# Kernel optimization log

Measured on AMD Instinct MI355X. Metric: run time of the kernel, lower is better.

The kernel has to match this reference:

```python
import jax, jax.numpy as jnp
import numpy as np

N, F_IN, H, HEADS = 50000, 128, 128, 4
C = H // HEADS
E = 800000


def layer_norm(x, w, b, eps=1e-5):
    mu = x.mean(-1, keepdims=True)
    var = ((x - mu) ** 2).mean(-1, keepdims=True)
    return (x - mu) * jax.lax.rsqrt(var + eps) * w + b


def gat_conv(x, src, dst, edge_attr, W, att_src, att_dst, W_edge, att_edge, bias):
    """PyG GATConv (concat=True, add_self_loops=True, fill_value='mean', edge_dim=H), eval mode."""
    n = x.shape[0]
    # self-loop edge_attr = mean of incoming edge attrs per node (PyG fill_value='mean')
    ones = jnp.ones((src.shape[0],), dtype=edge_attr.dtype)
    deg = jax.ops.segment_sum(ones, dst, n)
    loop_attr = jax.ops.segment_sum(edge_attr, dst, n) / jnp.maximum(deg, 1.0)[:, None]
    loop = jnp.arange(n, dtype=src.dtype)
    src = jnp.concatenate([src, loop])
    dst = jnp.concatenate([dst, loop])
    ea = jnp.concatenate([edge_attr, loop_attr], axis=0)  # [E+N, H]
    h = (x @ W).reshape(n, HEADS, C)                      # [N, heads, C]
    a_src = (h * att_src).sum(-1)                         # [N, heads]
    a_dst = (h * att_dst).sum(-1)
    e = (ea @ W_edge).reshape(-1, HEADS, C)
    a_edge = (e * att_edge).sum(-1)                       # [E+N, heads]
    alpha = jax.nn.leaky_relu(a_src[src] + a_dst[dst] + a_edge, 0.2)
    # segment softmax over destination neighborhoods
    m = jax.lax.stop_gradient(jax.ops.segment_max(alpha, dst, n))
    alpha = jnp.exp(alpha - m[dst])
    s = jax.ops.segment_sum(alpha, dst, n)
    alpha = alpha / (s[dst] + 1e-16)
    out = jax.ops.segment_sum(alpha[:, :, None] * h[src], dst, n)  # [N, heads, C]
    return out.reshape(n, H) + bias


def setup_inputs() -> dict:
    key = jax.random.key(0)
    ks = iter(jax.random.split(key, 40))
    def lin(k, i, o, s=0.05):
        return jax.random.normal(k, (i, o), jnp.float32) * s
    d = {}
    d["x"] = jax.random.normal(next(ks), (N, F_IN), jnp.float32)
    d["edge_time"] = jax.random.uniform(next(ks), (E,), jnp.float32)
    d["ip_w1"] = lin(next(ks), F_IN, 2 * H); d["ip_b1"] = jnp.zeros((2 * H,), jnp.float32)
    d["ip_ln_w"] = jnp.ones((2 * H,), jnp.float32); d["ip_ln_b"] = jnp.zeros((2 * H,), jnp.float32)
    d["ip_w2"] = lin(next(ks), 2 * H, H); d["ip_b2"] = jnp.zeros((H,), jnp.float32)
    d["pn_w"] = jnp.ones((H,), jnp.float32); d["pn_b"] = jnp.zeros((H,), jnp.float32)
    d["ta_w1"] = lin(next(ks), 1, H); d["ta_b1"] = jnp.zeros((H,), jnp.float32)
    d["ta_ln_w"] = jnp.ones((H,), jnp.float32); d["ta_ln_b"] = jnp.zeros((H,), jnp.float32)
    d["ta_w2"] = lin(next(ks), H, H); d["ta_b2"] = jnp.zeros((H,), jnp.float32)
    for p in ("g1", "g2"):
        d[p + "_w"] = lin(next(ks), H, H)
        d[p + "_att_src"] = jax.random.normal(next(ks), (HEADS, C), jnp.float32) * 0.05
        d[p + "_att_dst"] = jax.random.normal(next(ks), (HEADS, C), jnp.float32) * 0.05
        d[p + "_ew"] = lin(next(ks), H, H)
        d[p + "_att_edge"] = jax.random.normal(next(ks), (HEADS, C), jnp.float32) * 0.05
        d[p + "_b"] = jnp.zeros((H,), jnp.float32)
    d["n1_w"] = jnp.ones((H,), jnp.float32); d["n1_b"] = jnp.zeros((H,), jnp.float32)
    d["n2_w"] = jnp.ones((H,), jnp.float32); d["n2_b"] = jnp.zeros((H,), jnp.float32)
    d["edge_index"] = jax.random.randint(next(ks), (2, E), 0, N, jnp.int32)
    return d


def reference(x, edge_time, ip_w1, ip_b1, ip_ln_w, ip_ln_b, ip_w2, ip_b2, pn_w, pn_b,
              ta_w1, ta_b1, ta_ln_w, ta_ln_b, ta_w2, ta_b2,
              g1_w, g1_att_src, g1_att_dst, g1_ew, g1_att_edge, g1_b,
              g2_w, g2_att_src, g2_att_dst, g2_ew, g2_att_edge, g2_b,
              n1_w, n1_b, n2_w, n2_b, edge_index):
    src, dst = edge_index[0], edge_index[1]
    # input projection: Linear -> ReLU -> LayerNorm -> (Dropout eval) -> Linear
    h = jax.nn.relu(x @ ip_w1 + ip_b1)
    h = layer_norm(h, ip_ln_w, ip_ln_b)
    h = h @ ip_w2 + ip_b2
    h = jnp.clip(jax.nn.relu(layer_norm(h, pn_w, pn_b)), -10.0, 10.0)
    # temporal attention MLP on edge times -> per-edge edge_attr [E, H]
    tw = edge_time[:, None] @ ta_w1 + ta_b1
    tw = jax.nn.relu(layer_norm(tw, ta_ln_w, ta_ln_b))
    tw = jnp.clip(jnp.tanh(tw @ ta_w2 + ta_b2), -3.0, 3.0)
    # GAT layer 1 (single chunk => residual + clamp, mean over 1 chunk is identity)
    g = gat_conv(h, src, dst, tw, g1_w, g1_att_src, g1_att_dst, g1_ew, g1_att_edge, g1_b) + h
    g = jax.nn.elu(layer_norm(jnp.clip(g, -10.0, 10.0), n1_w, n1_b))
    # GAT layer 2
    g2 = gat_conv(g, src, dst, tw, g2_w, g2_att_src, g2_att_dst, g2_ew, g2_att_edge, g2_b) + g
    return jax.nn.elu(layer_norm(jnp.clip(g2, -10.0, 10.0), n2_w, n2_b))
```

## Files before the change

kernel.cpp:

```cpp
#include <hip/hip_runtime.h>

typedef unsigned short u16;
typedef __attribute__((ext_vector_type(8))) short bf8_t;
typedef __attribute__((ext_vector_type(4))) float f4_t;

constexpr int NN   = 50000;
constexpr int NE   = 800000;
constexpr int TBLN = 2048;
constexpr int MB64 = (NN + 63) / 64;
constexpr int FB   = NE / 256;

__device__ __forceinline__ u16 f2b(float f) {
  unsigned u = __float_as_uint(f);
  unsigned r = u + 0x7fffu + ((u >> 16) & 1u);
  return (u16)(r >> 16);
}
__device__ __forceinline__ u16 f2h(float f) {
  _Float16 h = (_Float16)f;
  return __builtin_bit_cast(unsigned short, h);
}
__device__ __forceinline__ float h2f(u16 v) {
  _Float16 h = __builtin_bit_cast(_Float16, v);
  return (float)h;
}
__device__ __forceinline__ unsigned packh(float a, float b) {
  return (unsigned)f2h(a) | ((unsigned)f2h(b) << 16);
}
__device__ __forceinline__ float blo(unsigned u) { return __uint_as_float(u << 16); }
__device__ __forceinline__ float bhi(unsigned u) { return __uint_as_float(u & 0xffff0000u); }
__device__ __forceinline__ float wred64(float v) {
#pragma unroll
  for (int o = 32; o; o >>= 1) v += __shfl_xor(v, o);
  return v;
}
__device__ __forceinline__ bf8_t ldv(const u16* p) { return *(const bf8_t*)p; }
__device__ __forceinline__ f4_t mfma16(bf8_t a, bf8_t b, f4_t c) {
  return __builtin_amdgcn_mfma_f32_16x16x32_bf16(a, b, c, 0, 0, 0);
}

__global__ __launch_bounds__(256) void prep_k(
    const float* __restrict__ ew1, const float* __restrict__ ate1,
    const float* __restrict__ ew2, const float* __restrict__ ate2,
    float* __restrict__ V,
    const float* __restrict__ w1, const float* __restrict__ w2,
    const float* __restrict__ gw1, const float* __restrict__ gw2,
    u16* __restrict__ w1t, u16* __restrict__ w2t,
    u16* __restrict__ g1wt, u16* __restrict__ g2wt,
    const int* __restrict__ dstv, int* __restrict__ deg,
    const float* __restrict__ x, u16* __restrict__ x16) {
  const int bid = blockIdx.x, t = threadIdx.x;
  if (bid == 0) {
#pragma unroll
    for (int rep = 0; rep < 2; ++rep) {
      int idx = t + rep * 256;
      int k = idx >> 2, hd = idx & 3;
      float s1 = 0.f, s2 = 0.f;
      for (int c = 0; c < 32; ++c) {
        s1 += ew1[k * 128 + hd * 32 + c] * ate1[hd * 32 + c];
        s2 += ew2[k * 128 + hd * 32 + c] * ate2[hd * 32 + c];
      }
      V[k * 8 + hd] = s1;
      V[k * 8 + 4 + hd] = s2;
    }
  } else if (bid <= 384) {
    int idx = (bid - 1) * 256 + t;
    if (idx < 32768) {
      int r = idx >> 8, c = idx & 255;
      w1t[c * 128 + r] = f2b(w1[idx]);
    } else if (idx < 65536) {
      int k = idx - 32768;
      int r = k >> 7, c = k & 127;
      w2t[c * 256 + r] = f2b(w2[k]);
    } else if (idx < 81920) {
      int k = idx - 65536;
      int r = k >> 7, c = k & 127;
      g1wt[c * 128 + r] = f2b(gw1[k]);
    } else {
      int k = idx - 81920;
      int r = k >> 7, c = k & 127;
      g2wt[c * 128 + r] = f2b(gw2[k]);
    }
  } else if (bid <= 384 + FB) {
    int e = (bid - 385) * 256 + t;
    if (e < NE) atomicAdd(&deg[dstv[e]], 1);
  } else {
    int idx = (bid - 385 - FB) * 256 + t;
    size_t e8 = (size_t)idx * 8;
    const float4 a = *(const float4*)(x + e8);
    const float4 b = *(const float4*)(x + e8 + 4);
    uint4 o;
    o.x = (unsigned)f2b(a.x) | ((unsigned)f2b(a.y) << 16);
    o.y = (unsigned)f2b(a.z) | ((unsigned)f2b(a.w) << 16);
    o.z = (unsigned)f2b(b.x) | ((unsigned)f2b(b.y) << 16);
    o.w = (unsigned)f2b(b.z) | ((unsigned)f2b(b.w) << 16);
    *(uint4*)(x16 + e8) = o;
  }
}

__global__ __launch_bounds__(128) void build_table(
    const float* __restrict__ taw1, const float* __restrict__ tab1,
    const float* __restrict__ talnw, const float* __restrict__ talnb,
    const float* __restrict__ taw2, const float* __restrict__ tab2,
    const float* __restrict__ V, float* __restrict__ tbl) {
  const int j = threadIdx.x;
  const int wv = j >> 6, ln = j & 63;
  const float t = (float)blockIdx.x / (float)(TBLN - 1);
  __shared__ float part[4];
  __shared__ float ush[128];
  __shared__ float pacc[16];
  float v = t * taw1[j] + tab1[j];
  float s = wred64(v), sq = wred64(v * v);
  if (ln == 0) { part[wv * 2] = s; part[wv * 2 + 1] = sq; }
  __syncthreads();
  float S = part[0] + part[2], SQ = part[1] + part[3];
  float mu = S * (1.f / 128.f);
  float var = SQ * (1.f / 128.f) - mu * mu;
  float rstd = rsqrtf(var + 1e-5f);
  float u = fmaxf((v - mu) * rstd * talnw[j] + talnb[j], 0.f);
  ush[j] = u;
  __syncthreads();
  float acc = 0.f;
  for (int k = 0; k < 128; ++k) acc += ush[k] * taw2[k * 128 + j];
  float w = tanhf(acc + tab2[j]);
  w = fminf(fmaxf(w, -3.f), 3.f);
#pragma unroll
  for (int p = 0; p < 8; ++p) {
    float z = wred64(w * V[j * 8 + p]);
    if (ln == 0) pacc[wv * 8 + p] = z;
  }
  __syncthreads();
  if (j < 8) tbl[blockIdx.x * 8 + j] = pacc[j] + pacc[8 + j];
}

__global__ __launch_bounds__(512) void scan1(const int* __restrict__ deg,
                                             int* __restrict__ indptr,
                                             int* __restrict__ blks) {
  const int t = threadIdx.x;
  const int i = blockIdx.x * 512 + t;
  int v = (i < NN) ? deg[i] : 0;
  const int lane = t & 63, wv = t >> 6;
  int x = v;
#pragma unroll
  for (int o = 1; o < 64; o <<= 1) {
    int y = __shfl_up(x, o);
    if (lane >= o) x += y;
  }
  __shared__ int ws[8];
  if (lane == 63) ws[wv] = x;
  __syncthreads();
  if (t < 8) {
    int y = ws[t];
#pragma unroll
    for (int o = 1; o < 8; o <<= 1) {
      int z = __shfl_up(y, o);
      if (t >= o) y += z;
    }
    ws[t] = y;
  }
  __syncthreads();
  int excl = wv ? ws[wv - 1] : 0;
  x += excl;
  if (i < NN) indptr[i + 1] = x;
  if (t == 511) blks[blockIdx.x] = x;
}
__global__ void scan2(int* __restrict__ blks, int nb) {
  const int t = threadIdx.x;
  int v = (t < nb) ? blks[t] : 0;
  const int lane = t & 63, wv = t >> 6;
  int x = v;
#pragma unroll
  for (int o = 1; o < 64; o <<= 1) {
    int y = __shfl_up(x, o);
    if (lane >= o) x += y;
  }
  __shared__ int ws[2];
  if (lane == 63) ws[wv] = x;
  __syncthreads();
  if (wv == 1) x += ws[0];
  if (t < nb) blks[t] = x - v;
}
__global__ __launch_bounds__(512) void scan3(int* __restrict__ indptr,
                                             const int* __restrict__ blks,
                                             const int* __restrict__ deg,
                                             int* __restrict__ cursor) {
  const int i = blockIdx.x * 512 + threadIdx.x;
  if (i < NN) {
    int v = indptr[i + 1] + blks[blockIdx.x];
    indptr[i + 1] = v;
    cursor[i] = v - deg[i];
  }
  if (i == 0) indptr[0] = 0;
}

__device__ void fill_body(int fb, const int* __restrict__ srcv,
                          const int* __restrict__ dstv,
                          const float* __restrict__ etime,
                          const float* __restrict__ tbl,
                          int* __restrict__ cursor,
                          u16* __restrict__ recs) {
  const int e = fb * 256 + threadIdx.x;
  if (e >= NE) return;
  int d = dstv[e];
  int pos = atomicAdd(&cursor[d], 1);
  float t = etime[e];
  t = fminf(fmaxf(t, 0.f), 1.f);
  float fpos = t * (float)(TBLN - 1);
  int i0 = (int)fpos;
  if (i0 > TBLN - 2) i0 = TBLN - 2;
  float fr = fpos - (float)i0;
  const float4* r = (const float4*)(tbl + i0 * 8);
  float4 a0 = r[0], a1 = r[1], b0 = r[2], b1 = r[3];
  float4 o1, o2;
  o1.x = a0.x + fr * (b0.x - a0.x); o1.y = a0.y + fr * (b0.y - a0.y);
  o1.z = a0.z + fr * (b0.z - a0.z); o1.w = a0.w + fr * (b0.w - a0.w);
  o2.x = a1.x + fr * (b1.x - a1.x); o2.y = a1.y + fr * (b1.y - a1.y);
  o2.z = a1.z + fr * (b1.z - a1.z); o2.w = a1.w + fr * (b1.w - a1.w);
  u16* rp = recs + (size_t)pos * 16;
  uint4 w;
  w.x = (unsigned)srcv[e];
  w.y = packh(o1.x, o1.y);
  w.z = packh(o1.z, o1.w);
  w.w = packh(o2.x, o2.y);
  *(uint4*)rp = w;
  *(unsigned*)(rp + 8) = packh(o2.z, o2.w);
}

__device__ void ip_body(int ipb, char* smem,
                        const u16* __restrict__ x16, const u16* __restrict__ w1t,
                        const float* __restrict__ b1, const float* __restrict__ ln1w,
                        const float* __restrict__ ln1b, const u16* __restrict__ w2t,
                        const float* __restrict__ b2, const float* __restrict__ pnw,
                        const float* __restrict__ pnb, u16* __restrict__ h16) {
  u16* h1n = (u16*)smem;
  u16* h2n = h1n;
  float* partS = (float*)(smem + 33792);
  float* partQ = (float*)(smem + 33792 + 1024);

  const int t = threadIdx.x;
  const int w = t >> 6, lane = t & 63, q = lane >> 4, l15 = lane & 15;
  const int rowbase = ipb * 64;

  f4_t acc[4][4];
#pragma unroll
  for (int mt = 0; mt < 4; ++mt)
#pragma unroll
    for (int nt = 0; nt < 4; ++nt) acc[mt][nt] = (f4_t){0.f, 0.f, 0.f, 0.f};
#pragma unroll
  for (int kst = 0; kst < 4; ++kst) {
    int k0 = kst * 32 + q * 8;
    bf8_t a[4];
#pragma unroll
    for (int mt = 0; mt < 4; ++mt) {
      int r = rowbase + mt * 16 + l15;
      if (r > NN - 1) r = NN - 1;
      a[mt] = ldv(x16 + (size_t)r * 128 + k0);
    }
#pragma unroll
    for (int nt = 0; nt < 4; ++nt) {
      int n = w * 64 + nt * 16 + l15;
      bf8_t b = ldv(w1t + n * 128 + k0);
#pragma unroll
      for (int mt = 0; mt < 4; ++mt)
        acc[mt][nt] = mfma16(a[mt], b, acc[mt][nt]);
    }
  }
#pragma unroll
  for (int nt = 0; nt < 4; ++nt) {
    float bb = b1[w * 64 + nt * 16 + l15];
#pragma unroll
    for (int mt = 0; mt < 4; ++mt)
#pragma unroll
      for (int r = 0; r < 4; ++r)
        acc[mt][nt][r] = fmaxf(acc[mt][nt][r] + bb, 0.f);
  }
  {
    float s[4][4], sq[4][4];
#pragma unroll
    for (int mt = 0; mt < 4; ++mt)
#pragma unroll
      for (int r = 0; r < 4; ++r) {
        float a0 = acc[mt][0][r], b0 = acc[mt][1][r], c0 = acc[mt][2][r], d0 = acc[mt][3][r];
        s[mt][r] = a0 + b0 + c0 + d0;
        sq[mt][r] = a0 * a0 + b0 * b0 + c0 * c0 + d0 * d0;
      }
#pragma unroll
    for (int o = 1; o < 16; o <<= 1)
#pragma unroll
      for (int mt = 0; mt < 4; ++mt)
#pragma unroll
        for (int r = 0; r < 4; ++r) {
          s[mt][r] += __shfl_xor(s[mt][r], o);
          sq[mt][r] += __shfl_xor(sq[mt][r], o);
        }
    if (l15 == 0) {
#pragma unroll
      for (int mt = 0; mt < 4; ++mt)
#pragma unroll
        for (int r = 0; r < 4; ++r) {
          int row = mt * 16 + q * 4 + r;
          partS[w * 64 + row] = s[mt][r];
          partQ[w * 64 + row] = sq[mt][r];
        }
    }
  }
  __syncthreads();
  {
    float lw[4], lb[4];
#pragma unroll
    for (int nt = 0; nt < 4; ++nt) {
      int col = w * 64 + nt * 16 + l15;
      lw[nt] = ln1w[col]; lb[nt] = ln1b[col];
    }
#pragma unroll
    for (int mt = 0; mt < 4; ++mt)
#pragma unroll
      for (int r = 0; r < 4; ++r) {
        int row = mt * 16 + q * 4 + r;
        float S = partS[row] + partS[64 + row] + partS[128 + row] + partS[192 + row];
        float Q = partQ[row] + partQ[64 + row] + partQ[128 + row] + partQ[192 + row];
        float mu = S * (1.f / 256.f);
        float var = Q * (1.f / 256.f) - mu * mu;
        float rstd = rsqrtf(var + 1e-5f);
#pragma unroll
        for (int nt = 0; nt < 4; ++nt) {
          int col = w * 64 + nt * 16 + l15;
          h1n[row * 264 + col] = f2b((acc[mt][nt][r] - mu) * rstd * lw[nt] + lb[nt]);
        }
      }
  }
  __syncthreads();
  f4_t acc2[4][2];
#pragma unroll
  for (int mt = 0; mt < 4; ++mt)
#pragma unroll
    for (int nt = 0; nt < 2; ++nt) acc2[mt][nt] = (f4_t){0.f, 0.f, 0.f, 0.f};
#pragma unroll
  for (int kst = 0; kst < 8; ++kst) {
    int k0 = kst * 32 + q * 8;
    bf8_t a[4];
#pragma unroll
    for (int mt = 0; mt < 4; ++mt)
      a[mt] = ldv(h1n + (mt * 16 + l15) * 264 + k0);
#pragma unroll
    for (int nt = 0; nt < 2; ++nt) {
      int n = w * 32 + nt * 16 + l15;
      bf8_t b = ldv(w2t + n * 256 + k0);
#pragma unroll
      for (int mt = 0; mt < 4; ++mt)
        acc2[mt][nt] = mfma16(a[mt], b, acc2[mt][nt]);
    }
  }
#pragma unroll
  for (int nt = 0; nt < 2; ++nt) {
    float bb = b2[w * 32 + nt * 16 + l15];
#pragma unroll
    for (int mt = 0; mt < 4; ++mt)
#pragma unroll
      for (int r = 0; r < 4; ++r)
        acc2[mt][nt][r] += bb;
  }
  {
    float s[4][4], sq[4][4];
#pragma unroll
    for (int mt = 0; mt < 4; ++mt)
#pragma unroll
      for (int r = 0; r < 4; ++r) {
        float a0 = acc2[mt][0][r], b0 = acc2[mt][1][r];
        s[mt][r] = a0 + b0;
        sq[mt][r] = a0 * a0 + b0 * b0;
      }
#pragma unroll
    for (int o = 1; o < 16; o <<= 1)
#pragma unroll
      for (int mt = 0; mt < 4; ++mt)
#pragma unroll
        for (int r = 0; r < 4; ++r) {
          s[mt][r] += __shfl_xor(s[mt][r], o);
          sq[mt][r] += __shfl_xor(sq[mt][r], o);
        }
    __syncthreads();
    if (l15 == 0) {
#pragma unroll
      for (int mt = 0; mt < 4; ++mt)
#pragma unroll
        for (int r = 0; r < 4; ++r) {
          int row = mt * 16 + q * 4 + r;
          partS[w * 64 + row] = s[mt][r];
          partQ[w * 64 + row] = sq[mt][r];
        }
    }
  }
  __syncthreads();
  {
    float lw[2], lb[2];
#pragma unroll
    for (int nt = 0; nt < 2; ++nt) {
      int col = w * 32 + nt * 16 + l15;
      lw[nt] = pnw[col]; lb[nt] = pnb[col];
    }
#pragma unroll
    for (int mt = 0; mt < 4; ++mt)
#pragma unroll
      for (int r = 0; r < 4; ++r) {
        int row = mt * 16 + q * 4 + r;
        float S = partS[row] + partS[64 + row] + partS[128 + row] + partS[192 + row];
        float Q = partQ[row] + partQ[64 + row] + partQ[128 + row] + partQ[192 + row];
        float mu = S * (1.f / 128.f);
        float var = Q * (1.f / 128.f) - mu * mu;
        float rstd = rsqrtf(var + 1e-5f);
#pragma unroll
        for (int nt = 0; nt < 2; ++nt) {
          int col = w * 32 + nt * 16 + l15;
          float v = (acc2[mt][nt][r] - mu) * rstd * lw[nt] + lb[nt];
          v = fminf(fmaxf(v, 0.f), 10.f);
          h2n[row * 128 + col] = f2b(v);
        }
      }
  }
  __syncthreads();
  {
    const int row = t >> 2, cb = (t & 3) * 32;
    int rg = rowbase + row;
    if (rg < NN) {
#pragma unroll
      for (int c = 0; c < 4; ++c) {
        uint4 v0 = *(const uint4*)(h2n + row * 128 + cb + c * 8);
        *(uint4*)(h16 + (size_t)rg * 128 + cb + c * 8) = v0;
      }
    }
  }
}

__global__ __launch_bounds__(256) void fillip_k(
    const int* srcv, const int* dstv, const float* etime, const float* tbl,
    int* cursor, u16* recs,
    const u16* x16, const u16* w1t, const float* b1, const float* ln1w,
    const float* ln1b, const u16* w2t, const float* b2, const float* pnw,
    const float* pnb, u16* h16) {
  __shared__ char smem[35840];
  const int bid = blockIdx.x;
  if (bid % 5 == 0) {
    ip_body(bid / 5, smem, x16, w1t, b1, ln1w, ln1b, w2t, b2, pnw, pnb, h16);
  } else {
    fill_body(bid - bid / 5 - 1, srcv, dstv, etime, tbl, cursor, recs);
  }
}

__global__ __launch_bounds__(256) void hp_mfma(
    const u16* __restrict__ feat16, const u16* __restrict__ wt,
    const float* __restrict__ attsrc, const float* __restrict__ attdst,
    u16* __restrict__ hp16, float* __restrict__ asrc, float* __restrict__ adst) {
  const int t = threadIdx.x;
  const int w = t >> 6, lane = t & 63, q = lane >> 4, l15 = lane & 15;
  const int rowbase = blockIdx.x * 64;
  f4_t acc[4][2];
#pragma unroll
  for (int mt = 0; mt < 4; ++mt)
#pragma unroll
    for (int nt = 0; nt < 2; ++nt) acc[mt][nt] = (f4_t){0.f, 0.f, 0.f, 0.f};
#pragma unroll
  for (int kst = 0; kst < 4; ++kst) {
    int k0 = kst * 32 + q * 8;
    bf8_t a[4];
#pragma unroll
    for (int mt = 0; mt < 4; ++mt) {
      int r = rowbase + mt * 16 + l15;
      if (r > NN - 1) r = NN - 1;
      a[mt] = ldv(feat16 + (size_t)r * 128 + k0);
    }
#pragma unroll
    for (int nt = 0; nt < 2; ++nt) {
      int n = w * 32 + nt * 16 + l15;
      bf8_t b = ldv(wt + n * 128 + k0);
#pragma unroll
      for (int mt = 0; mt < 4; ++mt)
        acc[mt][nt] = mfma16(a[mt], b, acc[mt][nt]);
    }
  }
  float ps[4][4], pd[4][4];
#pragma unroll
  for (int mt = 0; mt < 4; ++mt)
#pragma unroll
    for (int r = 0; r < 4; ++r) { ps[mt][r] = 0.f; pd[mt][r] = 0.f; }
#pragma unroll
  for (int mt = 0; mt < 4; ++mt)
#pragma unroll
    for (int nt = 0; nt < 2; ++nt) {
      int col = w * 32 + nt * 16 + l15;
      float as = attsrc[col], ad = attdst[col];
#pragma unroll
      for (int r = 0; r < 4; ++r) {
        int row = mt * 16 + q * 4 + r;
        int rg = rowbase + row;
        float v = acc[mt][nt][r];
        if (rg < NN) hp16[(size_t)rg * 128 + col] = f2b(v);
        ps[mt][r] += v * as;
        pd[mt][r] += v * ad;
      }
    }
#pragma unroll
  for (int o = 1; o < 16; o <<= 1)
#pragma unroll
    for (int mt = 0; mt < 4; ++mt)
#pragma unroll
      for (int r = 0; r < 4; ++r) {
        ps[mt][r] += __shfl_xor(ps[mt][r], o);
        pd[mt][r] += __shfl_xor(pd[mt][r], o);
      }
  if (l15 == 0) {
#pragma unroll
    for (int mt = 0; mt < 4; ++mt)
#pragma unroll
      for (int r = 0; r < 4; ++r) {
        int rg = rowbase + mt * 16 + q * 4 + r;
        if (rg < NN) {
          asrc[rg * 4 + w] = ps[mt][r];
          adst[rg * 4 + w] = pd[mt][r];
        }
      }
  }
}

template <int L, int FINAL>
__global__ __launch_bounds__(256) void agg_k(
    const int* __restrict__ indptr, const u16* __restrict__ recs,
    const float* __restrict__ asrc, const float* __restrict__ adst,
    const u16* __restrict__ hp16, const u16* __restrict__ feat16,
    const float* __restrict__ gbias, const float* __restrict__ lnw,
    const float* __restrict__ lnb, u16* __restrict__ gout16,
    float* __restrict__ out32) {
  const int wv = threadIdx.x >> 6, lane = threadIdx.x & 63;
  const int n = blockIdx.x * 4 + wv;
  if (n >= NN) return;
  const int s0 = indptr[n], s1 = indptr[n + 1];
  const int dg = s1 - s0;
  const int g = lane >> 4, sl = lane & 15, cb = sl * 8, hdB = sl >> 2;
  const float advB = adst[n * 4 + hdB];
  float ssp = 0.f, sap = 0.f;
  float acc[8];
#pragma unroll
  for (int i = 0; i < 8; ++i) acc[i] = 0.f;
  for (int base = s0; base < s1; base += 8) {
    int i0 = base + g, i1 = base + 4 + g;
    int j0 = i0 < s1 ? i0 : s1 - 1;
    int j1 = i1 < s1 ? i1 : s1 - 1;
    const u16* r0 = recs + (size_t)j0 * 16;
    const u16* r1 = recs + (size_t)j1 * 16;
    int sc0 = *(const int*)r0, sc1 = *(const int*)r1;
    float ae0 = h2f(r0[2 + 4 * L + hdB]);
    float ae1v = h2f(r1[2 + 4 * L + hdB]);
    float as0 = asrc[sc0 * 4 + hdB], as1 = asrc[sc1 * 4 + hdB];
    const uint4 row0 = *(const uint4*)(hp16 + (size_t)sc0 * 128 + cb);
    const uint4 row1 = *(const uint4*)(hp16 + (size_t)sc1 * 128 + cb);
    float l0 = as0 + advB + ae0; l0 = fmaxf(l0, 0.2f * l0);
    float l1 = as1 + advB + ae1v; l1 = fmaxf(l1, 0.2f * l1);
    float w0 = (i0 < s1) ? __expf(l0) : 0.f;
    float w1 = (i1 < s1) ? __expf(l1) : 0.f;
    ssp += w0 + w1;
    sap += ((i0 < s1) ? ae0 : 0.f) + ((i1 < s1) ? ae1v : 0.f);
    acc[0] += w0 * blo(row0.x) + w1 * blo(row1.x);
    acc[1] += w0 * bhi(row0.x) + w1 * bhi(row1.x);
    acc[2] += w0 * blo(row0.y) + w1 * blo(row1.y);
    acc[3] += w0 * bhi(row0.y) + w1 * bhi(row1.y);
    acc[4] += w0 * blo(row0.z) + w1 * blo(row1.z);
    acc[5] += w0 * bhi(row0.z) + w1 * bhi(row1.z);
    acc[6] += w0 * blo(row0.w) + w1 * blo(row1.w);
    acc[7] += w0 * bhi(row0.w) + w1 * bhi(row1.w);
  }
#pragma unroll
  for (int i = 0; i < 8; ++i) {
    acc[i] += __shfl_xor(acc[i], 16);
    acc[i] += __shfl_xor(acc[i], 32);
  }
  ssp += __shfl_xor(ssp, 16); ssp += __shfl_xor(ssp, 32);
  sap += __shfl_xor(sap, 16); sap += __shfl_xor(sap, 32);
  const float degf = (float)(dg > 0 ? dg : 1);
  float asnB = asrc[n * 4 + hdB];
  float la = asnB + advB + sap / degf;
  la = fmaxf(la, 0.2f * la);
  float wsf = __expf(la);
  float inv = 1.f / (ssp + wsf + 1e-16f);
  const uint4 rs4 = *(const uint4*)(hp16 + (size_t)n * 128 + cb);
  const uint4 rr4 = *(const uint4*)(feat16 + (size_t)n * 128 + cb);
  const float4 gb0 = *(const float4*)(gbias + cb);
  const float4 gb1 = *(const float4*)(gbias + cb + 4);
  float v[8];
  v[0] = (acc[0] + wsf * blo(rs4.x)) * inv + gb0.x + blo(rr4.x);
  v[1] = (acc[1] + wsf * bhi(rs4.x)) * inv + gb0.y + bhi(rr4.x);
  v[2] = (acc[2] + wsf * blo(rs4.y)) * inv + gb0.z + blo(rr4.y);
  v[3] = (acc[3] + wsf * bhi(rs4.y)) * inv + gb0.w + bhi(rr4.y);
  v[4] = (acc[4] + wsf * blo(rs4.z)) * inv + gb1.x + blo(rr4.z);
  v[5] = (acc[5] + wsf * bhi(rs4.z)) * inv + gb1.y + bhi(rr4.z);
  v[6] = (acc[6] + wsf * blo(rs4.w)) * inv + gb1.z + blo(rr4.w);
  v[7] = (acc[7] + wsf * bhi(rs4.w)) * inv + gb1.w + bhi(rr4.w);
  float sum = 0.f, sq = 0.f;
#pragma unroll
  for (int i = 0; i < 8; ++i) {
    v[i] = fminf(fmaxf(v[i], -10.f), 10.f);
    sum += v[i]; sq += v[i] * v[i];
  }
#pragma unroll
  for (int o = 1; o < 16; o <<= 1) {
    sum += __shfl_xor(sum, o);
    sq += __shfl_xor(sq, o);
  }
  float mu = sum * (1.f / 128.f);
  float var = sq * (1.f / 128.f) - mu * mu;
  float rstd = rsqrtf(var + 1e-5f);
  const float4 lw0 = *(const float4*)(lnw + cb);
  const float4 lw1 = *(const float4*)(lnw + cb + 4);
  const float4 lb0 = *(const float4*)(lnb + cb);
  const float4 lb1 = *(const float4*)(lnb + cb + 4);
  float y[8];
  y[0] = (v[0] - mu) * rstd * lw0.x + lb0.x;
  y[1] = (v[1] - mu) * rstd * lw0.y + lb0.y;
  y[2] = (v[2] - mu) * rstd * lw0.z + lb0.z;
  y[3] = (v[3] - mu) * rstd * lw0.w + lb0.w;
  y[4] = (v[4] - mu) * rstd * lw1.x + lb1.x;
  y[5] = (v[5] - mu) * rstd * lw1.y + lb1.y;
  y[6] = (v[6] - mu) * rstd * lw1.z + lb1.z;
  y[7] = (v[7] - mu) * rstd * lw1.w + lb1.w;
#pragma unroll
  for (int i = 0; i < 8; ++i) y[i] = y[i] > 0.f ? y[i] : expm1f(y[i]);
  if (g == 0) {
    if (FINAL) {
      float4 o0 = {y[0], y[1], y[2], y[3]};
      float4 o1 = {y[4], y[5], y[6], y[7]};
      *(float4*)(out32 + (size_t)n * 128 + cb) = o0;
      *(float4*)(out32 + (size_t)n * 128 + cb + 4) = o1;
    } else {
      uint4 o;
      o.x = (unsigned)f2b(y[0]) | ((unsigned)f2b(y[1]) << 16);
      o.y = (unsigned)f2b(y[2]) | ((unsigned)f2b(y[3]) << 16);
      o.z = (unsigned)f2b(y[4]) | ((unsigned)f2b(y[5]) << 16);
      o.w = (unsigned)f2b(y[6]) | ((unsigned)f2b(y[7]) << 16);
      *(uint4*)(gout16 + (size_t)n * 128 + cb) = o;
    }
  }
}

extern "C" void kernel_launch(void* const* d_in, const int* in_sizes, int n_in,
                              void* d_out, int out_size, void* d_ws, size_t ws_size,
                              hipStream_t stream) {
  const float* x      = (const float*)d_in[0];
  const float* etime  = (const float*)d_in[1];
  const float* ip_w1  = (const float*)d_in[2];
  const float* ip_b1  = (const float*)d_in[3];
  const float* ip_lnw = (const float*)d_in[4];
  const float* ip_lnb = (const float*)d_in[5];
  const float* ip_w2  = (const float*)d_in[6];
  const float* ip_b2  = (const float*)d_in[7];
  const float* pn_w   = (const float*)d_in[8];
  const float* pn_b   = (const float*)d_in[9];
  const float* ta_w1  = (const float*)d_in[10];
  const float* ta_b1  = (const float*)d_in[11];
  const float* ta_lnw = (const float*)d_in[12];
  const float* ta_lnb = (const float*)d_in[13];
  const float* ta_w2  = (const float*)d_in[14];
  const float* ta_b2  = (const float*)d_in[15];
  const float* g1_w   = (const float*)d_in[16];
  const float* g1_as  = (const float*)d_in[17];
  const float* g1_ad  = (const float*)d_in[18];
  const float* g1_ew  = (const float*)d_in[19];
  const float* g1_ae  = (const float*)d_in[20];
  const float* g1_b   = (const float*)d_in[21];
  const float* g2_w   = (const float*)d_in[22];
  const float* g2_as  = (const float*)d_in[23];
  const float* g2_ad  = (const float*)d_in[24];
  const float* g2_ew  = (const float*)d_in[25];
  const float* g2_ae  = (const float*)d_in[26];
  const float* g2_b   = (const float*)d_in[27];
  const float* n1_w   = (const float*)d_in[28];
  const float* n1_b   = (const float*)d_in[29];
  const float* n2_w   = (const float*)d_in[30];
  const float* n2_b   = (const float*)d_in[31];
  const int* eidx     = (const int*)d_in[32];
  const int* srcv = eidx;
  const int* dstv = eidx + NE;

  char* p = (char*)d_ws;
  auto carve = [&](size_t bytes) -> char* {
    char* r = p;
    p += (bytes + 255) & ~(size_t)255;
    return r;
  };
  u16*   h16    = (u16*)carve((size_t)NN * 128 * 2);
  u16*   g16    = (u16*)carve((size_t)NN * 128 * 2);
  u16*   hp16   = (u16*)carve((size_t)NN * 128 * 2);
  float* asrc   = (float*)carve((size_t)NN * 4 * 4);
  float* adst   = (float*)carve((size_t)NN * 4 * 4);
  u16*   recs   = (u16*)carve((size_t)NE * 32);
  int*   deg    = (int*)carve((size_t)NN * 4);
  int*   indptr = (int*)carve((size_t)(NN + 1) * 4);
  int*   cursor = (int*)carve((size_t)NN * 4);
  int*   blks   = (int*)carve(512 * 4);
  float* V      = (float*)carve(128 * 8 * 4);
  float* tbl    = (float*)carve((size_t)TBLN * 8 * 4);
  u16*   w1t    = (u16*)carve(128 * 256 * 2);
  u16*   w2t    = (u16*)carve(256 * 128 * 2);
  u16*   g1wt   = (u16*)carve(128 * 128 * 2);
  u16*   g2wt   = (u16*)carve(128 * 128 * 2);
  u16*   x16    = (u16*)g16;

  hipMemsetAsync(deg, 0, (size_t)NN * 4, stream);

  const int SCB = (NN + 511) / 512;

  prep_k<<<1 + 384 + FB + FB, 256, 0, stream>>>(g1_ew, g1_ae, g2_ew, g2_ae, V,
                                                ip_w1, ip_w2, g1_w, g2_w,
                                                w1t, w2t, g1wt, g2wt, dstv, deg,
                                                x, x16);
  build_table<<<TBLN, 128, 0, stream>>>(ta_w1, ta_b1, ta_lnw, ta_lnb, ta_w2, ta_b2, V, tbl);
  scan1<<<SCB, 512, 0, stream>>>(deg, indptr, blks);
  scan2<<<1, 128, 0, stream>>>(blks, SCB);
  scan3<<<SCB, 512, 0, stream>>>(indptr, blks, deg, cursor);
  fillip_k<<<MB64 + FB, 256, 0, stream>>>(srcv, dstv, etime, tbl, cursor, recs,
                                          x16, w1t, ip_b1, ip_lnw, ip_lnb, w2t, ip_b2,
                                          pn_w, pn_b, h16);
  hp_mfma<<<MB64, 256, 0, stream>>>(h16, g1wt, g1_as, g1_ad, hp16, asrc, adst);
  agg_k<0, 0><<<NN / 4, 256, 0, stream>>>(indptr, recs, asrc, adst, hp16, h16,
                                          g1_b, n1_w, n1_b, g16, nullptr);
  hp_mfma<<<MB64, 256, 0, stream>>>(g16, g2wt, g2_as, g2_ad, hp16, asrc, adst);
  agg_k<1, 1><<<NN / 4, 256, 0, stream>>>(indptr, recs, asrc, adst, hp16, g16,
                                          g2_b, n2_w, n2_b, nullptr, (float*)d_out);
}
```

Before: 389.7 us.

## Fuse GAT linear projections into input-projection and layer-1 aggregation kernels

Removes both standalone hp_mfma launches. The layer-1 projection (h·W1 plus the attention logits) now runs as MFMA inside the input-projection blocks, reading h from shared memory whose row stride is padded to 136 elements. The layer-2 projection is computed per node inside the layer-1 aggregation kernel with scalar FMAs and a butterfly shuffle reduction, writing to separate hp16b/asrc2/adst2 buffers. This saves two launches and the re-read of h and g from global memory, but adds heavy scalar ALU and weight-load work per node (each wave loads a 128x128 weight tile) inside the latency-bound aggregation kernel.

Result: slower. 406.9 us (+4.4%).

```diff
diff --git a/kernel.cpp b/kernel.cpp
--- a/kernel.cpp
+++ b/kernel.cpp
@@ -230,7 +230,10 @@
                         const float* __restrict__ b1, const float* __restrict__ ln1w,
                         const float* __restrict__ ln1b, const u16* __restrict__ w2t,
                         const float* __restrict__ b2, const float* __restrict__ pnw,
-                        const float* __restrict__ pnb, u16* __restrict__ h16) {
+                        const float* __restrict__ pnb, u16* __restrict__ h16,
+                        const u16* __restrict__ g1wt, const float* __restrict__ attsrc,
+                        const float* __restrict__ attdst, u16* __restrict__ hp16,
+                        float* __restrict__ asrc, float* __restrict__ adst) {
   u16* h1n = (u16*)smem;
   u16* h2n = h1n;
   float* partS = (float*)(smem + 33792);
@@ -413,7 +416,7 @@
           int col = w * 32 + nt * 16 + l15;
           float v = (acc2[mt][nt][r] - mu) * rstd * lw[nt] + lb[nt];
           v = fminf(fmaxf(v, 0.f), 10.f);
-          h2n[row * 128 + col] = f2b(v);
+          h2n[row * 136 + col] = f2b(v);
         }
       }
   }
@@ -424,9 +427,74 @@
     if (rg < NN) {
 #pragma unroll
       for (int c = 0; c < 4; ++c) {
-        uint4 v0 = *(const uint4*)(h2n + row * 128 + cb + c * 8);
+        uint4 v0 = *(const uint4*)(h2n + row * 136 + cb + c * 8);
         *(uint4*)(h16 + (size_t)rg * 128 + cb + c * 8) = v0;
       }
+    }
+  }
+  f4_t acc3[4][2];
+#pragma unroll
+  for (int mt = 0; mt < 4; ++mt)
+#pragma unroll
+    for (int nt = 0; nt < 2; ++nt) acc3[mt][nt] = (f4_t){0.f, 0.f, 0.f, 0.f};
+#pragma unroll
+  for (int kst = 0; kst < 4; ++kst) {
+    int k0 = kst * 32 + q * 8;
+    bf8_t a[4];
+#pragma unroll
+    for (int mt = 0; mt < 4; ++mt)
+      a[mt] = ldv(h2n + (mt * 16 + l15) * 136 + k0);
+#pragma unroll
+    for (int nt = 0; nt < 2; ++nt) {
+      int n = w * 32 + nt * 16 + l15;
+      bf8_t b = ldv(g1wt + n * 128 + k0);
+#pragma unroll
+      for (int mt = 0; mt < 4; ++mt)
+        acc3[mt][nt] = mfma16(a[mt], b, acc3[mt][nt]);
+    }
+  }
+  {
+    float ps[4][4], pd[4][4];
+#pragma unroll
+    for (int mt = 0; mt < 4; ++mt)
+#pragma unroll
+      for (int r = 0; r < 4; ++r) { ps[mt][r] = 0.f; pd[mt][r] = 0.f; }
+#pragma unroll
+    for (int mt = 0; mt < 4; ++mt)
+#pragma unroll
+      for (int nt = 0; nt < 2; ++nt) {
+        int col = w * 32 + nt * 16 + l15;
+        float as = attsrc[col], ad = attdst[col];
+#pragma unroll
+        for (int r = 0; r < 4; ++r) {
+          int row = mt * 16 + q * 4 + r;
+          int rg = rowbase + row;
+          float v = acc3[mt][nt][r];
+          if (rg < NN) hp16[(size_t)rg * 128 + col] = f2b(v);
+          ps[mt][r] += v * as;
+          pd[mt][r] += v * ad;
+        }
+      }
+#pragma unroll
+    for (int o = 1; o < 16; o <<= 1)
+#pragma unroll
+      for (int mt = 0; mt < 4; ++mt)
+#pragma unroll
+        for (int r = 0; r < 4; ++r) {
+          ps[mt][r] += __shfl_xor(ps[mt][r], o);
+          pd[mt][r] += __shfl_xor(pd[mt][r], o);
+        }
+    if (l15 == 0) {
+#pragma unroll
+      for (int mt = 0; mt < 4; ++mt)
+#pragma unroll
+        for (int r = 0; r < 4; ++r) {
+          int rg = rowbase + mt * 16 + q * 4 + r;
+          if (rg < NN) {
+            asrc[rg * 4 + w] = ps[mt][r];
+            adst[rg * 4 + w] = pd[mt][r];
+          }
+        }
     }
   }
 }
@@ -436,88 +504,16 @@
     int* cursor, u16* recs,
     const u16* x16, const u16* w1t, const float* b1, const float* ln1w,
     const float* ln1b, const u16* w2t, const float* b2, const float* pnw,
-    const float* pnb, u16* h16) {
+    const float* pnb, u16* h16,
+    const u16* g1wt, const float* g1as, const float* g1ad,
+    u16* hp16, float* asrc, float* adst) {
   __shared__ char smem[35840];
   const int bid = blockIdx.x;
   if (bid % 5 == 0) {
-    ip_body(bid / 5, smem, x16, w1t, b1, ln1w, ln1b, w2t, b2, pnw, pnb, h16);
+    ip_body(bid / 5, smem, x16, w1t, b1, ln1w, ln1b, w2t, b2, pnw, pnb, h16,
+            g1wt, g1as, g1ad, hp16, asrc, adst);
   } else {
     fill_body(bid - bid / 5 - 1, srcv, dstv, etime, tbl, cursor, recs);
-  }
-}
-
-__global__ __launch_bounds__(256) void hp_mfma(
-    const u16* __restrict__ feat16, const u16* __restrict__ wt,
-    const float* __restrict__ attsrc, const float* __restrict__ attdst,
-    u16* __restrict__ hp16, float* __restrict__ asrc, float* __restrict__ adst) {
-  const int t = threadIdx.x;
-  const int w = t >> 6, lane = t & 63, q = lane >> 4, l15 = lane & 15;
-  const int rowbase = blockIdx.x * 64;
-  f4_t acc[4][2];
-#pragma unroll
-  for (int mt = 0; mt < 4; ++mt)
-#pragma unroll
-    for (int nt = 0; nt < 2; ++nt) acc[mt][nt] = (f4_t){0.f, 0.f, 0.f, 0.f};
-#pragma unroll
-  for (int kst = 0; kst < 4; ++kst) {
-    int k0 = kst * 32 + q * 8;
-    bf8_t a[4];
-#pragma unroll
-    for (int mt = 0; mt < 4; ++mt) {
-      int r = rowbase + mt * 16 + l15;
-      if (r > NN - 1) r = NN - 1;
-      a[mt] = ldv(feat16 + (size_t)r * 128 + k0);
-    }
-#pragma unroll
-    for (int nt = 0; nt < 2; ++nt) {
-      int n = w * 32 + nt * 16 + l15;
-      bf8_t b = ldv(wt + n * 128 + k0);
-#pragma unroll
-      for (int mt = 0; mt < 4; ++mt)
-        acc[mt][nt] = mfma16(a[mt], b, acc[mt][nt]);
-    }
-  }
-  float ps[4][4], pd[4][4];
-#pragma unroll
-  for (int mt = 0; mt < 4; ++mt)
-#pragma unroll
-    for (int r = 0; r < 4; ++r) { ps[mt][r] = 0.f; pd[mt][r] = 0.f; }
-#pragma unroll
-  for (int mt = 0; mt < 4; ++mt)
-#pragma unroll
-    for (int nt = 0; nt < 2; ++nt) {
-      int col = w * 32 + nt * 16 + l15;
-      float as = attsrc[col], ad = attdst[col];
-#pragma unroll
-      for (int r = 0; r < 4; ++r) {
-        int row = mt * 16 + q * 4 + r;
-        int rg = rowbase + row;
-        float v = acc[mt][nt][r];
-        if (rg < NN) hp16[(size_t)rg * 128 + col] = f2b(v);
-        ps[mt][r] += v * as;
-        pd[mt][r] += v * ad;
-      }
-    }
-#pragma unroll
-  for (int o = 1; o < 16; o <<= 1)
-#pragma unroll
-    for (int mt = 0; mt < 4; ++mt)
-#pragma unroll
-      for (int r = 0; r < 4; ++r) {
-        ps[mt][r] += __shfl_xor(ps[mt][r], o);
-        pd[mt][r] += __shfl_xor(pd[mt][r], o);
-      }
-  if (l15 == 0) {
-#pragma unroll
-    for (int mt = 0; mt < 4; ++mt)
-#pragma unroll
-      for (int r = 0; r < 4; ++r) {
-        int rg = rowbase + mt * 16 + q * 4 + r;
-        if (rg < NN) {
-          asrc[rg * 4 + w] = ps[mt][r];
-          adst[rg * 4 + w] = pd[mt][r];
-        }
-      }
   }
 }
 
@@ -528,7 +524,10 @@
     const u16* __restrict__ hp16, const u16* __restrict__ feat16,
     const float* __restrict__ gbias, const float* __restrict__ lnw,
     const float* __restrict__ lnb, u16* __restrict__ gout16,
-    float* __restrict__ out32) {
+    float* __restrict__ out32,
+    const u16* __restrict__ g2wt, const float* __restrict__ as2,
+    const float* __restrict__ ad2, u16* __restrict__ hp16b,
+    float* __restrict__ asrc2, float* __restrict__ adst2) {
   const int wv = threadIdx.x >> 6, lane = threadIdx.x & 63;
   const int n = blockIdx.x * 4 + wv;
   if (n >= NN) return;
@@ -622,19 +621,81 @@
   y[7] = (v[7] - mu) * rstd * lw1.w + lb1.w;
 #pragma unroll
   for (int i = 0; i < 8; ++i) y[i] = y[i] > 0.f ? y[i] : expm1f(y[i]);
-  if (g == 0) {
-    if (FINAL) {
+  if (FINAL) {
+    if (g == 0) {
       float4 o0 = {y[0], y[1], y[2], y[3]};
       float4 o1 = {y[4], y[5], y[6], y[7]};
       *(float4*)(out32 + (size_t)n * 128 + cb) = o0;
       *(float4*)(out32 + (size_t)n * 128 + cb + 4) = o1;
-    } else {
+    }
+  } else {
+    if (g == 0) {
       uint4 o;
       o.x = (unsigned)f2b(y[0]) | ((unsigned)f2b(y[1]) << 16);
       o.y = (unsigned)f2b(y[2]) | ((unsigned)f2b(y[3]) << 16);
       o.z = (unsigned)f2b(y[4]) | ((unsigned)f2b(y[5]) << 16);
       o.w = (unsigned)f2b(y[6]) | ((unsigned)f2b(y[7]) << 16);
       *(uint4*)(gout16 + (size_t)n * 128 + cb) = o;
+    }
+    float t0[16], t1[16];
+#pragma unroll
+    for (int c = 0; c < 16; ++c) {
+      const uint4 a4 = *(const uint4*)(g2wt + (g * 32 + c) * 128 + cb);
+      const uint4 b4 = *(const uint4*)(g2wt + (g * 32 + 16 + c) * 128 + cb);
+      t0[c] = y[0] * blo(a4.x) + y[1] * bhi(a4.x) + y[2] * blo(a4.y) + y[3] * bhi(a4.y)
+            + y[4] * blo(a4.z) + y[5] * bhi(a4.z) + y[6] * blo(a4.w) + y[7] * bhi(a4.w);
+      t1[c] = y[0] * blo(b4.x) + y[1] * bhi(b4.x) + y[2] * blo(b4.y) + y[3] * bhi(b4.y)
+            + y[4] * blo(b4.z) + y[5] * bhi(b4.z) + y[6] * blo(b4.w) + y[7] * bhi(b4.w);
+    }
+#pragma unroll
+    for (int c = 0; c < 8; ++c) {
+      float lo = t0[c], hi = t0[c + 8];
+      float mine = (sl & 8) ? hi : lo, send = (sl & 8) ? lo : hi;
+      t0[c] = mine + __shfl_xor(send, 8);
+      lo = t1[c]; hi = t1[c + 8];
+      mine = (sl & 8) ? hi : lo; send = (sl & 8) ? lo : hi;
+      t1[c] = mine + __shfl_xor(send, 8);
+    }
+#pragma unroll
+    for (int c = 0; c < 4; ++c) {
+      float lo = t0[c], hi = t0[c + 4];
+      float mine = (sl & 4) ? hi : lo, send = (sl & 4) ? lo : hi;
+      t0[c] = mine + __shfl_xor(send, 4);
+      lo = t1[c]; hi = t1[c + 4];
+      mine = (sl & 4) ? hi : lo; send = (sl & 4) ? lo : hi;
+      t1[c] = mine + __shfl_xor(send, 4);
+    }
+#pragma unroll
+    for (int c = 0; c < 2; ++c) {
+      float lo = t0[c], hi = t0[c + 2];
+      float mine = (sl & 2) ? hi : lo, send = (sl & 2) ? lo : hi;
+      t0[c] = mine + __shfl_xor(send, 2);
+      lo = t1[c]; hi = t1[c + 2];
+      mine = (sl & 2) ? hi : lo; send = (sl & 2) ? lo : hi;
+      t1[c] = mine + __shfl_xor(send, 2);
+    }
+    {
+      float lo = t0[0], hi = t0[1];
+      float mine = (sl & 1) ? hi : lo, send = (sl & 1) ? lo : hi;
+      t0[0] = mine + __shfl_xor(send, 1);
+      lo = t1[0]; hi = t1[1];
+      mine = (sl & 1) ? hi : lo; send = (sl & 1) ? lo : hi;
+      t1[0] = mine + __shfl_xor(send, 1);
+    }
+    const float s0v = t0[0], s1v = t1[0];
+    const int col0 = g * 32 + sl, col1 = col0 + 16;
+    hp16b[(size_t)n * 128 + col0] = f2b(s0v);
+    hp16b[(size_t)n * 128 + col1] = f2b(s1v);
+    float pa = s0v * as2[col0] + s1v * as2[col1];
+    float pdv = s0v * ad2[col0] + s1v * ad2[col1];
+#pragma unroll
+    for (int o = 1; o < 16; o <<= 1) {
+      pa += __shfl_xor(pa, o);
+      pdv += __shfl_xor(pdv, o);
+    }
+    if (sl == 0) {
+      asrc2[n * 4 + g] = pa;
+      adst2[n * 4 + g] = pdv;
     }
   }
 }
@@ -687,8 +748,11 @@
   u16*   h16    = (u16*)carve((size_t)NN * 128 * 2);
   u16*   g16    = (u16*)carve((size_t)NN * 128 * 2);
   u16*   hp16   = (u16*)carve((size_t)NN * 128 * 2);
+  u16*   hp16b  = (u16*)carve((size_t)NN * 128 * 2);
   float* asrc   = (float*)carve((size_t)NN * 4 * 4);
   float* adst   = (float*)carve((size_t)NN * 4 * 4);
+  float* asrc2  = (float*)carve((size_t)NN * 4 * 4);
+  float* adst2  = (float*)carve((size_t)NN * 4 * 4);
   u16*   recs   = (u16*)carve((size_t)NE * 32);
   int*   deg    = (int*)carve((size_t)NN * 4);
   int*   indptr = (int*)carve((size_t)(NN + 1) * 4);
@@ -716,11 +780,13 @@
   scan3<<<SCB, 512, 0, stream>>>(indptr, blks, deg, cursor);
   fillip_k<<<MB64 + FB, 256, 0, stream>>>(srcv, dstv, etime, tbl, cursor, recs,
                                           x16, w1t, ip_b1, ip_lnw, ip_lnb, w2t, ip_b2,
-                                          pn_w, pn_b, h16);
-  hp_mfma<<<MB64, 256, 0, stream>>>(h16, g1wt, g1_as, g1_ad, hp16, asrc, adst);
+                                          pn_w, pn_b, h16,
+                                          g1wt, g1_as, g1_ad, hp16, asrc, adst);
   agg_k<0, 0><<<NN / 4, 256, 0, stream>>>(indptr, recs, asrc, adst, hp16, h16,
-                                          g1_b, n1_w, n1_b, g16, nullptr);
-  hp_mfma<<<MB64, 256, 0, stream>>>(g16, g2wt, g2_as, g2_ad, hp16, asrc, adst);
-  agg_k<1, 1><<<NN / 4, 256, 0, stream>>>(indptr, recs, asrc, adst, hp16, g16,
-                                          g2_b, n2_w, n2_b, nullptr, (float*)d_out);
-}
+                                          g1_b, n1_w, n1_b, g16, nullptr,
+                                          g2wt, g2_as, g2_ad, hp16b, asrc2, adst2);
+  agg_k<1, 1><<<NN / 4, 256, 0, stream>>>(indptr, recs, asrc2, adst2, hp16b, g16,
+                                          g2_b, n2_w, n2_b, nullptr, (float*)d_out,
+                                          nullptr, nullptr, nullptr, nullptr,
+                                          nullptr, nullptr);
+}
```
